# Kernel optimization log

Measured on AMD Instinct MI355X. Metric: run time of the kernel, lower is better.

## Reference

```python
import jax, jax.numpy as jnp
import numpy as np


def setup_inputs() -> dict:
    key = jax.random.key(0)
    k1, k2, k3 = jax.random.split(key, 3)
    B, CIN, T, K = 64, 64, 1, 4096
    COUT, F = 64, 4
    L = F * K  # 16384; gather index space per (b, o)
    x = jax.random.normal(k1, (B, CIN, T, K), dtype=jnp.float32)
    upsample_params = jax.random.normal(k2, (CIN, COUT, F), dtype=jnp.float32)
    indices = jax.random.randint(k3, (L,), 0, L, dtype=jnp.int64 if jax.config.jax_enable_x64 else jnp.int32)
    return {"x": x, "upsample_params": upsample_params, "indices": indices}


def reference(x, upsample_params, indices):
    # x: [B, Cin, T, K]; params: [Cin, Cout, 4] -> res: [B, Cout, 4, K]
    res = jnp.einsum('bitk,iof->bofk', x, upsample_params)
    B, O = res.shape[0], res.shape[1]
    L = indices.shape[0]  # == 4*K
    # torch: flatten + index_select with per-(b,o) offset == gather along last axis
    flat = res.reshape(B, O, L)
    out = jnp.take(flat, indices, axis=2)
    return out.reshape(B, O, 1, L)
```

## Files before the change

### kernel.cpp

```cpp
#include <hip/hip_runtime.h>


typedef __attribute__((ext_vector_type(8))) short short8;
typedef __attribute__((ext_vector_type(4))) float floatx4;

#define NB    64
#define CIN   64
#define COUT  64
#define KDIM  4096
#define LDIM  16384
#define BXS   264
#define ITERS 8

__device__ __forceinline__ unsigned short f2bf(float f) {
  union { float f; unsigned u; } v; v.f = f;
  unsigned r = v.u + 0x7FFFu + ((v.u >> 16) & 1u);
  return (unsigned short)(r >> 16);
}

__global__ __launch_bounds__(256) void transpose_bf16(const float* __restrict__ x,
                                                      unsigned short* __restrict__ xt) {
  __shared__ float tile[64 * 65];
  const int t = threadIdx.x;
  const int b = blockIdx.y;
  const int k0 = blockIdx.x * 64;
  const float4* x4 = (const float4*)x;
#pragma unroll
  for (int p = 0; p < 4; ++p) {
    int i  = p * 16 + (t >> 4);
    int kq = t & 15;
    float4 v = x4[(size_t)(b * CIN + i) * (KDIM / 4) + (k0 >> 2) + kq];
    tile[i * 65 + kq * 4 + 0] = v.x;
    tile[i * 65 + kq * 4 + 1] = v.y;
    tile[i * 65 + kq * 4 + 2] = v.z;
    tile[i * 65 + kq * 4 + 3] = v.w;
  }
  __syncthreads();
  unsigned int* xt32 = (unsigned int*)xt;
  const int ip = (t & 31) * 2;
#pragma unroll
  for (int p = 0; p < 8; ++p) {
    int k = p * 8 + (t >> 5);
    unsigned lo = f2bf(tile[ip * 65 + k]);
    unsigned hi = f2bf(tile[(ip + 1) * 65 + k]);
    xt32[((size_t)b * KDIM + k0 + k) * (CIN / 2) + (ip >> 1)] = lo | (hi << 16);
  }
}

__global__ __launch_bounds__(256) void gemm_gather(const unsigned short* __restrict__ xt,
                                                   const float* __restrict__ params,
                                                   const int* __restrict__ idx,
                                                   float* __restrict__ out) {
  __shared__ __align__(16) unsigned short Bx[64 * BXS];
  const int t = threadIdx.x;
  const int b = blockIdx.y;
  const int w = t >> 6;
  const int lane = t & 63;
  const int quad = lane >> 4;
  const int lane15 = lane & 15;

  short8 afrag[8];
  {
    const int o = w * 16 + lane15;
#pragma unroll
    for (int kt = 0; kt < 8; ++kt) {
      short8 a;
#pragma unroll
      for (int j = 0; j < 8; ++j) {
        int s = kt * 32 + quad * 8 + j;
        int i = s & 63, g = s >> 6;
        a[j] = (short)f2bf(params[(i * COUT + o) * 4 + g]);
      }
      afrag[kt] = a;
    }
  }

  const int u = t & 3;
  const int lrow = t >> 2;
  const uint4 zero4 = make_uint4(0u, 0u, 0u, 0u);

  for (int it = 0; it < ITERS; ++it) {
    const int l_base = (blockIdx.x * ITERS + it) * 64;

    const int iv = idx[l_base + lrow];
    const int kp = iv & (KDIM - 1);
    const int fp = iv >> 12;
    const uint4* xrow = (const uint4*)(xt + ((size_t)b * KDIM + kp) * CIN);
    uint4 d0 = xrow[2 * u];
    uint4 d1 = xrow[2 * u + 1];
#pragma unroll
    for (int g = 0; g < 4; ++g) {
      uint4 w0 = (g == fp) ? d0 : zero4;
      uint4 w1 = (g == fp) ? d1 : zero4;
      *(uint4*)&Bx[lrow * BXS + g * 64 + (2 * u) * 8]     = w0;
      *(uint4*)&Bx[lrow * BXS + g * 64 + (2 * u + 1) * 8] = w1;
    }
    __syncthreads();

    floatx4 acc[4] = {floatx4{0.f,0.f,0.f,0.f}, floatx4{0.f,0.f,0.f,0.f},
                      floatx4{0.f,0.f,0.f,0.f}, floatx4{0.f,0.f,0.f,0.f}};
#pragma unroll
    for (int kt = 0; kt < 8; ++kt) {
#pragma unroll
      for (int nt = 0; nt < 4; ++nt) {
        short8 bf = *(const short8*)&Bx[(nt * 16 + lane15) * BXS + kt * 32 + quad * 8];
        acc[nt] = __builtin_amdgcn_mfma_f32_16x16x32_bf16(afrag[kt], bf, acc[nt], 0, 0, 0);
      }
    }

#pragma unroll
    for (int nt = 0; nt < 4; ++nt) {
      const int l = l_base + nt * 16 + lane15;
#pragma unroll
      for (int r = 0; r < 4; ++r) {
        const int o = w * 16 + quad * 4 + r;
        out[((size_t)(b * COUT + o)) * LDIM + l] = acc[nt][r];
      }
    }
    __syncthreads();
  }
}

extern "C" void kernel_launch(void* const* d_in, const int* in_sizes, int n_in,
                              void* d_out, int out_size, void* d_ws, size_t ws_size,
                              hipStream_t stream) {
  const float* x      = (const float*)d_in[0];
  const float* params = (const float*)d_in[1];
  const int*   idx    = (const int*)d_in[2];
  float* out = (float*)d_out;
  unsigned short* xt = (unsigned short*)d_ws;

  transpose_bf16<<<dim3(KDIM / 64, NB), 256, 0, stream>>>(x, xt);
  gemm_gather<<<dim3(LDIM / 64 / ITERS, NB), 256, 0, stream>>>(xt, params, idx, out);
}
```

Before: 345.6 us.

## Keep gathered B fragments in registers and prepack bf16 A fragments

Drops the LDS staging of the zero-padded gathered tile. Each wave now loads its gathered x row directly into MFMA B-fragment registers and selects zero or data per k-tile based on the gather's f index. A separate small kernel prepacks the params into bf16 fragment layout, so every block loads them with vector reads instead of converting scattered floats. Each wave holds all 4 M-tiles (32 short8 registers), which raises register pressure, and the next gather is prefetched one iteration ahead.

After: 408.1 us. +18.1%, slower.

```diff
diff --git a/kernel.cpp b/kernel.cpp
--- a/kernel.cpp
+++ b/kernel.cpp
@@ -9,8 +9,8 @@
 #define COUT  64
 #define KDIM  4096
 #define LDIM  16384
-#define BXS   264
 #define ITERS 8
+#define XT_BYTES ((size_t)NB * KDIM * CIN * 2)
 
 __device__ __forceinline__ unsigned short f2bf(float f) {
   union { float f; unsigned u; } v; v.f = f;
@@ -47,77 +47,83 @@
   }
 }
 
-__global__ __launch_bounds__(256) void gemm_gather(const unsigned short* __restrict__ xt,
-                                                   const float* __restrict__ params,
+__global__ __launch_bounds__(256) void prepack_afrag(const float* __restrict__ p,
+                                                     unsigned short* __restrict__ pb) {
+  const int t = blockIdx.x * 256 + threadIdx.x;
+  const int lane = t & 63;
+  const int mk = t >> 6;
+  const int mt = mk >> 3, kt = mk & 7;
+  const int o = mt * 16 + (lane & 15);
+  const int quad = lane >> 4;
+#pragma unroll
+  for (int j = 0; j < 8; ++j) {
+    int s = kt * 32 + quad * 8 + j;
+    int i = s & 63, g = s >> 6;
+    pb[t * 8 + j] = f2bf(p[(i * COUT + o) * 4 + g]);
+  }
+}
+
+__global__ __launch_bounds__(256, 2) void gemm_reg(const unsigned short* __restrict__ xt,
+                                                   const unsigned short* __restrict__ pb,
                                                    const int* __restrict__ idx,
                                                    float* __restrict__ out) {
-  __shared__ __align__(16) unsigned short Bx[64 * BXS];
   const int t = threadIdx.x;
   const int b = blockIdx.y;
   const int w = t >> 6;
   const int lane = t & 63;
+  const int lane15 = lane & 15;
   const int quad = lane >> 4;
-  const int lane15 = lane & 15;
 
-  short8 afrag[8];
+  short8 af[4][8];
   {
-    const int o = w * 16 + lane15;
+    const short8* pbv = (const short8*)pb;
+#pragma unroll
+    for (int mt = 0; mt < 4; ++mt)
+#pragma unroll
+      for (int kt = 0; kt < 8; ++kt)
+        af[mt][kt] = pbv[(mt * 8 + kt) * 64 + lane];
+  }
+
+  const int l0 = blockIdx.x * (4 * 16 * ITERS) + w * 16;
+  const unsigned short* xb = xt + (size_t)b * KDIM * CIN;
+
+  int iv = idx[l0 + lane15];
+  const short8* row = (const short8*)(xb + (size_t)(iv & (KDIM - 1)) * CIN);
+  int fp = iv >> 12;
+  short8 ev = row[quad];
+  short8 ov = row[4 + quad];
+
+  const short8 z8 = {0, 0, 0, 0, 0, 0, 0, 0};
+
+  for (int it = 0; it < ITERS; ++it) {
+    const int fpc = fp;
+    const short8 evc = ev, ovc = ov;
+    if (it < ITERS - 1) {
+      int iv2 = idx[l0 + (it + 1) * 64 + lane15];
+      row = (const short8*)(xb + (size_t)(iv2 & (KDIM - 1)) * CIN);
+      fp = iv2 >> 12;
+      ev = row[quad];
+      ov = row[4 + quad];
+    }
+
+    floatx4 acc[4] = {floatx4{0.f, 0.f, 0.f, 0.f}, floatx4{0.f, 0.f, 0.f, 0.f},
+                      floatx4{0.f, 0.f, 0.f, 0.f}, floatx4{0.f, 0.f, 0.f, 0.f}};
 #pragma unroll
     for (int kt = 0; kt < 8; ++kt) {
-      short8 a;
+      const short8 h = (kt & 1) ? ovc : evc;
+      const short8 bf = (fpc == (kt >> 1)) ? h : z8;
 #pragma unroll
-      for (int j = 0; j < 8; ++j) {
-        int s = kt * 32 + quad * 8 + j;
-        int i = s & 63, g = s >> 6;
-        a[j] = (short)f2bf(params[(i * COUT + o) * 4 + g]);
-      }
-      afrag[kt] = a;
-    }
-  }
-
-  const int u = t & 3;
-  const int lrow = t >> 2;
-  const uint4 zero4 = make_uint4(0u, 0u, 0u, 0u);
-
-  for (int it = 0; it < ITERS; ++it) {
-    const int l_base = (blockIdx.x * ITERS + it) * 64;
-
-    const int iv = idx[l_base + lrow];
-    const int kp = iv & (KDIM - 1);
-    const int fp = iv >> 12;
-    const uint4* xrow = (const uint4*)(xt + ((size_t)b * KDIM + kp) * CIN);
-    uint4 d0 = xrow[2 * u];
-    uint4 d1 = xrow[2 * u + 1];
-#pragma unroll
-    for (int g = 0; g < 4; ++g) {
-      uint4 w0 = (g == fp) ? d0 : zero4;
-      uint4 w1 = (g == fp) ? d1 : zero4;
-      *(uint4*)&Bx[lrow * BXS + g * 64 + (2 * u) * 8]     = w0;
-      *(uint4*)&Bx[lrow * BXS + g * 64 + (2 * u + 1) * 8] = w1;
-    }
-    __syncthreads();
-
-    floatx4 acc[4] = {floatx4{0.f,0.f,0.f,0.f}, floatx4{0.f,0.f,0.f,0.f},
-                      floatx4{0.f,0.f,0.f,0.f}, floatx4{0.f,0.f,0.f,0.f}};
-#pragma unroll
-    for (int kt = 0; kt < 8; ++kt) {
-#pragma unroll
-      for (int nt = 0; nt < 4; ++nt) {
-        short8 bf = *(const short8*)&Bx[(nt * 16 + lane15) * BXS + kt * 32 + quad * 8];
-        acc[nt] = __builtin_amdgcn_mfma_f32_16x16x32_bf16(afrag[kt], bf, acc[nt], 0, 0, 0);
-      }
+      for (int mt = 0; mt < 4; ++mt)
+        acc[mt] = __builtin_amdgcn_mfma_f32_16x16x32_bf16(af[mt][kt], bf, acc[mt], 0, 0, 0);
     }
 
+    const int l = l0 + it * 64 + lane15;
+    float* ob = out + (size_t)b * COUT * LDIM + l;
 #pragma unroll
-    for (int nt = 0; nt < 4; ++nt) {
-      const int l = l_base + nt * 16 + lane15;
+    for (int mt = 0; mt < 4; ++mt)
 #pragma unroll
-      for (int r = 0; r < 4; ++r) {
-        const int o = w * 16 + quad * 4 + r;
-        out[((size_t)(b * COUT + o)) * LDIM + l] = acc[nt][r];
-      }
-    }
-    __syncthreads();
+      for (int r = 0; r < 4; ++r)
+        ob[(size_t)(mt * 16 + quad * 4 + r) * LDIM] = acc[mt][r];
   }
 }
 
@@ -129,7 +135,9 @@
   const int*   idx    = (const int*)d_in[2];
   float* out = (float*)d_out;
   unsigned short* xt = (unsigned short*)d_ws;
+  unsigned short* pb = (unsigned short*)((char*)d_ws + XT_BYTES);
 
   transpose_bf16<<<dim3(KDIM / 64, NB), 256, 0, stream>>>(x, xt);
-  gemm_gather<<<dim3(LDIM / 64 / ITERS, NB), 256, 0, stream>>>(xt, params, idx, out);
+  prepack_afrag<<<dim3(8), 256, 0, stream>>>(params, pb);
+  gemm_reg<<<dim3(LDIM / (64 * ITERS), NB), 256, 0, stream>>>(xt, pb, idx, out);
 }
```
